# Kernel tuning notes

Hardware: AMD Instinct MI355X
Metric: run time of the kernel (lower is better)

The kernel has to match this reference:

```python
import jax, jax.numpy as jnp
import numpy as np

N_QUBITS = 10
DIM = 1 << N_QUBITS  # 1024

# Constant QFT matrix (PennyLane convention: F[j,k] = w^{jk}/sqrt(N), w = exp(2*pi*i/N),
# wire 0 = most significant bit). Symmetric, so state @ F == F @ state per sample.
_jk = (np.outer(np.arange(DIM), np.arange(DIM)) % DIM).astype(np.float64)
QFT_MAT = jnp.asarray((np.exp(2j * np.pi * _jk / DIM) / np.sqrt(DIM)).astype(np.complex64))


def _apply_1q(state, U, q):
    """Apply 2x2 gate U to wire q (wire 0 = MSB). state: [B, DIM] complex."""
    B = state.shape[0]
    left, right = 1 << q, 1 << (N_QUBITS - 1 - q)
    s = state.reshape(B, left, 2, right)
    s = jnp.einsum('ij,bajc->baic', U, s)
    return s.reshape(B, DIM)


def _apply_cnot(state, c, t):
    """CNOT with control c, target t (wire 0 = MSB)."""
    B = state.shape[0]
    a, b = (c, t) if c < t else (t, c)
    s = state.reshape(B, 1 << a, 2, 1 << (b - a - 1), 2, 1 << (N_QUBITS - 1 - b))
    ctrl_ax, tgt_ax = (2, 4) if c < t else (4, 2)
    s0 = jax.lax.index_in_dim(s, 0, ctrl_ax, keepdims=False)
    s1 = jax.lax.index_in_dim(s, 1, ctrl_ax, keepdims=False)
    ta = tgt_ax - 1 if tgt_ax > ctrl_ax else tgt_ax  # target axis after squeezing ctrl
    s1 = jnp.flip(s1, axis=ta)  # X on target when control == 1
    s = jnp.stack([s0, s1], axis=ctrl_ax)
    return s.reshape(B, DIM)


def _rx(t):
    c = jnp.cos(t / 2).astype(jnp.complex64)
    s = (-1j * jnp.sin(t / 2)).astype(jnp.complex64)
    return jnp.stack([jnp.stack([c, s]), jnp.stack([s, c])])


def _ry(t):
    c = jnp.cos(t / 2).astype(jnp.complex64)
    s = jnp.sin(t / 2).astype(jnp.complex64)
    return jnp.stack([jnp.stack([c, -s]), jnp.stack([s, c])])


def _rz(t):
    e = jnp.exp(-0.5j * t.astype(jnp.complex64))
    z = jnp.zeros((), jnp.complex64)
    return jnp.stack([jnp.stack([e, z]), jnp.stack([z, jnp.conj(e)])])


def _forward(x, weights):
    B = x.shape[0]
    # Pad/truncate is a no-op here (x already [B, DIM]); normalize as in the module.
    nrm = jnp.linalg.norm(x, axis=-1, keepdims=True)
    xn = x / jnp.maximum(nrm, 1e-8)
    state = xn.astype(jnp.complex64)  # AmplitudeEmbedding (already unit-norm)
    for q in range(N_QUBITS):
        state = _apply_1q(state, _rx(weights[q, 0]), q)
    for q in range(N_QUBITS):
        state = _apply_1q(state, _ry(weights[q, 1]), q)
    for q in range(N_QUBITS):
        state = _apply_1q(state, _rz(weights[q, 2]), q)
    for q in range(N_QUBITS):
        state = _apply_cnot(state, q, (q + 1) % N_QUBITS)
    for q in range(N_QUBITS):
        state = _apply_1q(state, _ry(weights[q, 3]), q)
    state = state @ QFT_MAT  # QFT (symmetric matrix)
    ex, ey, ez = [], [], []
    for q in range(N_QUBITS):
        s = state.reshape(B, 1 << q, 2, 1 << (N_QUBITS - 1 - q))
        s0, s1 = s[:, :, 0, :], s[:, :, 1, :]
        cross = jnp.sum(jnp.conj(s0) * s1, axis=(1, 2))
        ex.append(2.0 * jnp.real(cross))                # <X_q>
        ey.append(2.0 * jnp.imag(cross))                # <Y_q>
        ez.append(jnp.sum(jnp.abs(s0) ** 2 - jnp.abs(s1) ** 2, axis=(1, 2)))  # <Z_q>
    return jnp.stack(ex + ey + ez, axis=1).astype(jnp.float32)  # [B, 3*N_QUBITS]


def setup_inputs() -> dict:
    key = jax.random.key(0)
    kx, kw = jax.random.split(key)
    x = jax.random.normal(kx, (8192, 1024), dtype=jnp.float32)
    weights = jax.random.normal(kw, (10, 4), dtype=jnp.float32) * 0.01
    return {"x": x, "weights": weights}


def reference(x, weights):
    return _forward(x, weights)
```

## Files before the change

kernel.cpp:

```cpp
#include <hip/hip_runtime.h>


typedef _Float16 half2_t __attribute__((ext_vector_type(2)));

__device__ __forceinline__ unsigned pk16(float a, float b) {
    half2_t h; h[0] = (_Float16)a; h[1] = (_Float16)b;
    return __builtin_bit_cast(unsigned, h);
}
__device__ __forceinline__ float2 up16(unsigned u) {
    half2_t h = __builtin_bit_cast(half2_t, u);
    return make_float2((float)h[0], (float)h[1]);
}

__device__ __forceinline__ float lxor(float v, int e) {
    if (e == 0)
        return __builtin_bit_cast(float, __builtin_amdgcn_mov_dpp(
            __builtin_bit_cast(int, v), 0xB1, 0xF, 0xF, true));
    else if (e == 1)
        return __builtin_bit_cast(float, __builtin_amdgcn_mov_dpp(
            __builtin_bit_cast(int, v), 0x4E, 0xF, 0xF, true));
    else if (e == 2)
        return __builtin_bit_cast(float, __builtin_amdgcn_ds_swizzle(
            __builtin_bit_cast(int, v), (4 << 10) | 0x1F));
    else if (e == 3)
        return __builtin_bit_cast(float, __builtin_amdgcn_ds_swizzle(
            __builtin_bit_cast(int, v), (8 << 10) | 0x1F));
    else if (e == 4)
        return __builtin_bit_cast(float, __builtin_amdgcn_ds_swizzle(
            __builtin_bit_cast(int, v), (16 << 10) | 0x1F));
    else
        return __shfl_xor(v, 32);
}

__device__ __forceinline__ float wred(float v) {
    v += lxor(v, 0);
    v += lxor(v, 1);
    v += lxor(v, 2);
    v += lxor(v, 3);
    v += lxor(v, 4);
    v += lxor(v, 5);
    return v;
}

__device__ __forceinline__ int cnotrev(int k) {
    int m = (int)(__brev((unsigned)k) >> 22);
    #pragma unroll
    for (int q = 9; q >= 0; --q) {
        const int pc = (q == 9) ? 0 : 9 - q;
        const int pt = (q == 9) ? 9 : 8 - q;
        m ^= ((m >> pc) & 1) << pt;
    }
    return m;
}

__global__ __launch_bounds__(256) void fused_kernel(const float* __restrict__ w,
                                                    const float* __restrict__ x,
                                                    float* __restrict__ out)
{
    __shared__ float uu[10][8];
    __shared__ float ryc[10], rys[10];
    __shared__ __align__(16) unsigned scr[4][1024];
    const int tid = threadIdx.x;
    const int wv = tid >> 6, l = tid & 63;
    const int row = blockIdx.x * 4 + wv;
    unsigned* bw = scr[wv];

    if (tid < 10) {
        float t0 = w[tid*4 + 0] * 0.5f, t1 = w[tid*4 + 1] * 0.5f;
        float t2 = w[tid*4 + 2] * 0.5f, t3 = w[tid*4 + 3] * 0.5f;
        float s0, c0, s1, c1, s2, c2, s3, c3;
        __sincosf(t0, &s0, &c0);
        __sincosf(t1, &s1, &c1);
        __sincosf(t2, &s2, &c2);
        __sincosf(t3, &s3, &c3);
        uu[tid][0] =  c2*c1*c0 + s2*s1*s0;
        uu[tid][1] =  c2*s1*s0 - s2*c1*c0;
        uu[tid][2] = -(c2*s1*c0 + s2*c1*s0);
        uu[tid][3] =  s2*s1*c0 - c2*c1*s0;
        uu[tid][4] =  c2*s1*c0 + s2*c1*s0;
        uu[tid][5] =  s2*s1*c0 - c2*c1*s0;
        uu[tid][6] =  c2*c1*c0 + s2*s1*s0;
        uu[tid][7] =  s2*c1*c0 - c2*s1*s0;
        ryc[tid] = c3;
        rys[tid] = s3;
    }
    __syncthreads();

    const float* xr = x + (size_t)row * 1024 + l * 16;
    float4 v0 = ((const float4*)xr)[0];
    float4 v1 = ((const float4*)xr)[1];
    float4 v2 = ((const float4*)xr)[2];
    float4 v3 = ((const float4*)xr)[3];
    float ss = v0.x*v0.x + v0.y*v0.y + v0.z*v0.z + v0.w*v0.w
             + v1.x*v1.x + v1.y*v1.y + v1.z*v1.z + v1.w*v1.w
             + v2.x*v2.x + v2.y*v2.y + v2.z*v2.z + v2.w*v2.w
             + v3.x*v3.x + v3.y*v3.y + v3.z*v3.z + v3.w*v3.w;
    ss = wred(ss);
    const float scale = 0.03125f / fmaxf(sqrtf(ss), 1e-8f);

    float2 c[16];
    c[0]  = make_float2(v0.x*scale, 0.f); c[1]  = make_float2(v0.y*scale, 0.f);
    c[2]  = make_float2(v0.z*scale, 0.f); c[3]  = make_float2(v0.w*scale, 0.f);
    c[4]  = make_float2(v1.x*scale, 0.f); c[5]  = make_float2(v1.y*scale, 0.f);
    c[6]  = make_float2(v1.z*scale, 0.f); c[7]  = make_float2(v1.w*scale, 0.f);
    c[8]  = make_float2(v2.x*scale, 0.f); c[9]  = make_float2(v2.y*scale, 0.f);
    c[10] = make_float2(v2.z*scale, 0.f); c[11] = make_float2(v2.w*scale, 0.f);
    c[12] = make_float2(v3.x*scale, 0.f); c[13] = make_float2(v3.y*scale, 0.f);
    c[14] = make_float2(v3.z*scale, 0.f); c[15] = make_float2(v3.w*scale, 0.f);

    #pragma unroll
    for (int p = 0; p < 4; ++p) {
        const float* U = uu[9 - p];
        const float u00r = U[0], u00i = U[1], u01r = U[2], u01i = U[3];
        const float u10r = U[4], u10i = U[5], u11r = U[6], u11i = U[7];
        const int m = 1 << p;
        #pragma unroll
        for (int i = 0; i < 16; ++i) {
            if (i & m) continue;
            const int j = i | m;
            const float ar = c[i].x, ai = c[i].y, br = c[j].x, bi = c[j].y;
            c[i].x = u00r*ar - u00i*ai + u01r*br - u01i*bi;
            c[i].y = u00r*ai + u00i*ar + u01r*bi + u01i*br;
            c[j].x = u10r*ar - u10i*ai + u11r*br - u11i*bi;
            c[j].y = u10r*ai + u10i*ar + u11r*bi + u11i*br;
        }
    }
    #pragma unroll
    for (int e = 0; e < 6; ++e) {
        const float* U = uu[5 - e];
        const int mybit = (l >> e) & 1;
        const float car = mybit ? U[6] : U[0];
        const float cai = mybit ? U[7] : U[1];
        const float cbr = mybit ? U[4] : U[2];
        const float cbi = mybit ? U[5] : U[3];
        #pragma unroll
        for (int i = 0; i < 16; ++i) {
            const float fr = lxor(c[i].x, e);
            const float fi = lxor(c[i].y, e);
            const float ar = c[i].x, ai = c[i].y;
            c[i].x = car*ar - cai*ai + cbr*fr - cbi*fi;
            c[i].y = car*ai + cai*ar + cbr*fi + cbi*fr;
        }
    }

    #pragma unroll
    for (int j = 0; j < 8; ++j) {
        const int su = l*8 + (j ^ (l & 7));
        uint2 pv;
        pv.x = pk16(c[2*j].x,     c[2*j].y);
        pv.y = pk16(c[2*j + 1].x, c[2*j + 1].y);
        ((uint2*)bw)[su] = pv;
    }
    const int mb = cnotrev(l << 4);
    #pragma unroll
    for (int i = 0; i < 16; ++i) {
        const int m = mb ^ cnotrev(i);
        const int lm = m >> 4, um = (m >> 1) & 7, lo = m & 1;
        c[i] = up16(bw[(lm*8 + (um ^ (lm & 7)))*2 + lo]);
    }

    #pragma unroll
    for (int p = 0; p < 4; ++p) {
        const float cc = ryc[p], sv = rys[p];
        const int m = 1 << p;
        #pragma unroll
        for (int i = 0; i < 16; ++i) {
            if (i & m) continue;
            const int j = i | m;
            const float ar = c[i].x, ai = c[i].y, br = c[j].x, bi = c[j].y;
            c[i].x = cc*ar - sv*br;  c[i].y = cc*ai - sv*bi;
            c[j].x = sv*ar + cc*br;  c[j].y = sv*ai + cc*bi;
        }
    }
    #pragma unroll
    for (int e = 0; e < 6; ++e) {
        const float cc = ryc[4 + e], sv = rys[4 + e];
        const int mybit = (l >> e) & 1;
        const float sel = mybit ? sv : -sv;
        #pragma unroll
        for (int i = 0; i < 16; ++i) {
            const float fr = lxor(c[i].x, e);
            const float fi = lxor(c[i].y, e);
            c[i].x = cc*c[i].x + sel*fr;
            c[i].y = cc*c[i].y + sel*fi;
        }
    }

    {
        const float TC8[8] = { 1.f,  0.92387953f,  0.70710678f,  0.38268343f,
                               0.f, -0.38268343f, -0.70710678f, -0.92387953f };
        const float TS8[8] = { 0.f,  0.38268343f,  0.70710678f,  0.92387953f,
                               1.f,  0.92387953f,  0.70710678f,  0.38268343f };
        #pragma unroll
        for (int st = 1; st <= 4; ++st) {
            const int hf = 1 << (st - 1);
            #pragma unroll
            for (int i = 0; i < 16; ++i) {
                if (i & hf) continue;
                const int j = i | hf;
                const int tix = (i & (hf - 1)) << (4 - st);
                const float cwv = TC8[tix], swv = TS8[tix];
                const float tr = cwv*c[j].x - swv*c[j].y;
                const float ti = cwv*c[j].y + swv*c[j].x;
                const float ur = c[i].x, ui = c[i].y;
                c[i].x = ur + tr; c[i].y = ui + ti;
                c[j].x = ur - tr; c[j].y = ui - ti;
            }
        }
    }
    {
        const float CT[6][16] = {
          { 1.f,0.98078528f,0.92387953f,0.83146961f,0.70710678f,0.55557023f,0.38268343f,0.19509032f,
            0.f,-0.19509032f,-0.38268343f,-0.55557023f,-0.70710678f,-0.83146961f,-0.92387953f,-0.98078528f },
          { 1.f,0.99518473f,0.98078528f,0.95694034f,0.92387953f,0.88192126f,0.83146961f,0.77301045f,
            0.70710678f,0.63439328f,0.55557023f,0.47139674f,0.38268343f,0.29028468f,0.19509032f,0.09801714f },
          { 1.f,0.99879546f,0.99518473f,0.98917651f,0.98078528f,0.97003125f,0.95694034f,0.94154407f,
            0.92387953f,0.90398929f,0.88192126f,0.85772861f,0.83146961f,0.80320753f,0.77301045f,0.74095113f },
          { 1.f,0.99969882f,0.99879546f,0.99729046f,0.99518473f,0.99247953f,0.98917651f,0.98527764f,
            0.98078528f,0.97570213f,0.97003125f,0.96377607f,0.95694034f,0.94952818f,0.94154407f,0.93299280f },
          { 1.f,0.99992470f,0.99969882f,0.99932238f,0.99879546f,0.99811811f,0.99729046f,0.99631261f,
            0.99518473f,0.99390697f,0.99247953f,0.99090264f,0.98917651f,0.98730142f,0.98527764f,0.98310549f },
          { 1.f,0.99998118f,0.99992470f,0.99983058f,0.99969882f,0.99952942f,0.99932238f,0.99907773f,
            0.99879546f,0.99847559f,0.99811811f,0.99772307f,0.99729046f,0.99682030f,0.99631261f,0.99576742f } };
        const float ST[6][16] = {
          { 0.f,0.19509032f,0.38268343f,0.55557023f,0.70710678f,0.83146961f,0.92387953f,0.98078528f,
            1.f,0.98078528f,0.92387953f,0.83146961f,0.70710678f,0.55557023f,0.38268343f,0.19509032f },
          { 0.f,0.09801714f,0.19509032f,0.29028468f,0.38268343f,0.47139674f,0.55557023f,0.63439328f,
            0.70710678f,0.77301045f,0.83146961f,0.88192126f,0.92387953f,0.95694034f,0.98078528f,0.99518473f },
          { 0.f,0.04906767f,0.09801714f,0.14673047f,0.19509032f,0.24298018f,0.29028468f,0.33688985f,
            0.38268343f,0.42755509f,0.47139674f,0.51410274f,0.55557023f,0.59569930f,0.63439328f,0.67155895f },
          { 0.f,0.02454123f,0.04906767f,0.07356456f,0.09801714f,0.12241068f,0.14673047f,0.17096189f,
            0.19509032f,0.21910124f,0.24298018f,0.26671276f,0.29028468f,0.31368174f,0.33688985f,0.35989504f },
          { 0.f,0.01227154f,0.02454123f,0.03680722f,0.04906767f,0.06132074f,0.07356456f,0.08579731f,
            0.09801714f,0.11022221f,0.12241068f,0.13458071f,0.14673047f,0.15885814f,0.17096189f,0.18303989f },
          { 0.f,0.00613588f,0.01227154f,0.01840673f,0.02454123f,0.03067480f,0.03680722f,0.04293826f,
            0.04906767f,0.05519524f,0.06132074f,0.06744392f,0.07356456f,0.07968244f,0.08579731f,0.09190896f } };
        #pragma unroll
        for (int e2 = 0; e2 < 6; ++e2) {
            const int st = 5 + e2;
            const float astep = 6.28318530717958647f / (float)(1 << st);
            const int mybit = (l >> e2) & 1;
            const float sel = mybit ? -1.f : 1.f;
            float cb, sb;
            __sincosf(astep * 16.0f * (float)(l & ((1 << e2) - 1)), &sb, &cb);
            #pragma unroll
            for (int i = 0; i < 16; ++i) {
                const float cw = cb*CT[e2][i] - sb*ST[e2][i];
                const float sw = sb*CT[e2][i] + cb*ST[e2][i];
                const float pr = cw*c[i].x - sw*c[i].y;
                const float pi = cw*c[i].y + sw*c[i].x;
                const float vr = mybit ? pr : c[i].x;
                const float vi = mybit ? pi : c[i].y;
                const float fr = lxor(vr, e2);
                const float fi = lxor(vi, e2);
                c[i].x = fmaf(sel, vr, fr);
                c[i].y = fmaf(sel, vi, fi);
            }
        }
    }

    #pragma unroll
    for (int j = 0; j < 8; ++j) {
        const int su = l*8 + (j ^ (l & 7));
        uint2 pv;
        pv.x = pk16(c[2*j].x,     c[2*j].y);
        pv.y = pk16(c[2*j + 1].x, c[2*j + 1].y);
        ((uint2*)bw)[su] = pv;
    }

    float P2s = 0.f;
    #pragma unroll
    for (int i = 0; i < 16; ++i)
        P2s += c[i].x*c[i].x + c[i].y*c[i].y;

    float outv = 0.f;

    #pragma unroll
    for (int p = 0; p < 4; ++p) {
        const int m = 1 << p;
        const int q = 9 - p;
        float rr = 0.f, ii = 0.f, zz = 0.f;
        #pragma unroll
        for (int i = 0; i < 16; ++i) {
            if (i & m) continue;
            const int j = i | m;
            rr += c[i].x*c[j].x + c[i].y*c[j].y;
            ii += c[i].x*c[j].y - c[i].y*c[j].x;
            zz += (c[i].x*c[i].x + c[i].y*c[i].y) - (c[j].x*c[j].x + c[j].y*c[j].y);
        }
        rr = wred(rr);
        ii = wred(ii);
        zz = wred(zz);
        outv = (l == q)      ? 2.f*rr : outv;
        outv = (l == 10 + q) ? 2.f*ii : outv;
        outv = (l == 20 + q) ? zz     : outv;
    }

    #pragma unroll
    for (int e = 0; e < 6; ++e) {
        const int q = 5 - e;
        const int part = l ^ (1 << e);
        const int mybit = (l >> e) & 1;
        const float sgn = mybit ? -1.f : 1.f;
        const int j0 = mybit ? 4 : 0;
        float rr = 0.f, ii = 0.f;
        #pragma unroll
        for (int j = 0; j < 4; ++j) {
            const int su = part*8 + ((j0 + j) ^ (part & 7));
            const uint2 d = ((const uint2*)bw)[su];
            const float2 f01 = up16(d.x);
            const float2 f23 = up16(d.y);
            const float2 a0 = c[2*j],     a1 = c[2*j + 1];
            const float2 b0 = c[2*j + 8], b1 = c[2*j + 9];
            const float m0x = mybit ? b0.x : a0.x;
            const float m0y = mybit ? b0.y : a0.y;
            const float m1x = mybit ? b1.x : a1.x;
            const float m1y = mybit ? b1.y : a1.y;
            rr += m0x*f01.x + m0y*f01.y;
            ii += m0x*f01.y - m0y*f01.x;
            rr += m1x*f23.x + m1y*f23.y;
            ii += m1x*f23.y - m1y*f23.x;
        }
        const float rr_s = wred(rr);
        const float ii_s = wred(sgn * ii);
        const float zz_s = wred(sgn * P2s);
        outv = (l == q)      ? 2.f*rr_s : outv;
        outv = (l == 10 + q) ? 2.f*ii_s : outv;
        outv = (l == 20 + q) ? zz_s     : outv;
    }

    if (l < 30)
        out[(size_t)row * 30 + l] = outv;
}

extern "C" void kernel_launch(void* const* d_in, const int* in_sizes, int n_in,
                              void* d_out, int out_size, void* d_ws, size_t ws_size,
                              hipStream_t stream) {
    const float* x = (const float*)d_in[0];
    const float* w = (const float*)d_in[1];
    float* out = (float*)d_out;
    (void)d_ws; (void)ws_size;

    fused_kernel<<<2048, 256, 0, stream>>>(w, x, out);
}
```

Measured before the change: 145.8 us.

## Use fp32 LDS staging and cross-lane shuffles for high-qubit expectations

Replaces the fp16-packed shared-memory scratch with full fp32 float4 storage for the CNOT permutation, doubling LDS use per wave. Drops the second LDS store of the final state and instead computes the cross-lane X/Y expectation terms with DPP/swizzle lane exchanges over all 16 amplitudes. Because each lane pair is now counted twice, the factor of 2 is dropped. This removes LDS round trips and fp16 conversions at the cost of more shuffle instructions and higher LDS footprint, which may reduce occupancy.

```diff
diff --git a/kernel.cpp b/kernel.cpp
--- a/kernel.cpp
+++ b/kernel.cpp
@@ -1,16 +1,5 @@
 #include <hip/hip_runtime.h>
 
-
-typedef _Float16 half2_t __attribute__((ext_vector_type(2)));
-
-__device__ __forceinline__ unsigned pk16(float a, float b) {
-    half2_t h; h[0] = (_Float16)a; h[1] = (_Float16)b;
-    return __builtin_bit_cast(unsigned, h);
-}
-__device__ __forceinline__ float2 up16(unsigned u) {
-    half2_t h = __builtin_bit_cast(half2_t, u);
-    return make_float2((float)h[0], (float)h[1]);
-}
 
 __device__ __forceinline__ float lxor(float v, int e) {
     if (e == 0)
@@ -59,11 +48,11 @@
 {
     __shared__ float uu[10][8];
     __shared__ float ryc[10], rys[10];
-    __shared__ __align__(16) unsigned scr[4][1024];
+    __shared__ __align__(16) float scr[4][2048];
     const int tid = threadIdx.x;
     const int wv = tid >> 6, l = tid & 63;
     const int row = blockIdx.x * 4 + wv;
-    unsigned* bw = scr[wv];
+    float* bw = scr[wv];
 
     if (tid < 10) {
         float t0 = w[tid*4 + 0] * 0.5f, t1 = w[tid*4 + 1] * 0.5f;
@@ -146,17 +135,15 @@
     #pragma unroll
     for (int j = 0; j < 8; ++j) {
         const int su = l*8 + (j ^ (l & 7));
-        uint2 pv;
-        pv.x = pk16(c[2*j].x,     c[2*j].y);
-        pv.y = pk16(c[2*j + 1].x, c[2*j + 1].y);
-        ((uint2*)bw)[su] = pv;
+        ((float4*)bw)[su] = make_float4(c[2*j].x, c[2*j].y, c[2*j+1].x, c[2*j+1].y);
     }
     const int mb = cnotrev(l << 4);
     #pragma unroll
     for (int i = 0; i < 16; ++i) {
         const int m = mb ^ cnotrev(i);
         const int lm = m >> 4, um = (m >> 1) & 7, lo = m & 1;
-        c[i] = up16(bw[(lm*8 + (um ^ (lm & 7)))*2 + lo]);
+        const int su = lm*8 + (um ^ (lm & 7));
+        c[i] = ((const float2*)bw)[su*2 + lo];
     }
 
     #pragma unroll
@@ -259,15 +246,6 @@
         }
     }
 
-    #pragma unroll
-    for (int j = 0; j < 8; ++j) {
-        const int su = l*8 + (j ^ (l & 7));
-        uint2 pv;
-        pv.x = pk16(c[2*j].x,     c[2*j].y);
-        pv.y = pk16(c[2*j + 1].x, c[2*j + 1].y);
-        ((uint2*)bw)[su] = pv;
-    }
-
     float P2s = 0.f;
     #pragma unroll
     for (int i = 0; i < 16; ++i)
@@ -299,34 +277,22 @@
     #pragma unroll
     for (int e = 0; e < 6; ++e) {
         const int q = 5 - e;
-        const int part = l ^ (1 << e);
         const int mybit = (l >> e) & 1;
         const float sgn = mybit ? -1.f : 1.f;
-        const int j0 = mybit ? 4 : 0;
         float rr = 0.f, ii = 0.f;
         #pragma unroll
-        for (int j = 0; j < 4; ++j) {
-            const int su = part*8 + ((j0 + j) ^ (part & 7));
-            const uint2 d = ((const uint2*)bw)[su];
-            const float2 f01 = up16(d.x);
-            const float2 f23 = up16(d.y);
-            const float2 a0 = c[2*j],     a1 = c[2*j + 1];
-            const float2 b0 = c[2*j + 8], b1 = c[2*j + 9];
-            const float m0x = mybit ? b0.x : a0.x;
-            const float m0y = mybit ? b0.y : a0.y;
-            const float m1x = mybit ? b1.x : a1.x;
-            const float m1y = mybit ? b1.y : a1.y;
-            rr += m0x*f01.x + m0y*f01.y;
-            ii += m0x*f01.y - m0y*f01.x;
-            rr += m1x*f23.x + m1y*f23.y;
-            ii += m1x*f23.y - m1y*f23.x;
+        for (int i = 0; i < 16; ++i) {
+            const float fr = lxor(c[i].x, e);
+            const float fi = lxor(c[i].y, e);
+            rr += c[i].x*fr + c[i].y*fi;
+            ii += c[i].x*fi - c[i].y*fr;
         }
         const float rr_s = wred(rr);
         const float ii_s = wred(sgn * ii);
         const float zz_s = wred(sgn * P2s);
-        outv = (l == q)      ? 2.f*rr_s : outv;
-        outv = (l == 10 + q) ? 2.f*ii_s : outv;
-        outv = (l == 20 + q) ? zz_s     : outv;
+        outv = (l == q)      ? rr_s : outv;
+        outv = (l == 10 + q) ? ii_s : outv;
+        outv = (l == 20 + q) ? zz_s : outv;
     }
 
     if (l < 30)
```

Measured after the change: 142.6 us (median of 3 runs). 1.02x faster.
